# Optimization experiments

Measured on AMD Instinct MI355X. Metric: run time of the kernel, lower is better.

## Reference

```python
import jax, jax.numpy as jnp
import numpy as np

EPS = 1e-5
SLOPE = 0.2
K = 20
B, N = 8, 2048

def _lrelu(x):
    return jnp.where(x >= 0, x, SLOPE * x)

def _bn(x, g, b, m, v, axis):
    # eval-mode batchnorm with running stats
    shape = [1] * x.ndim
    shape[axis] = -1
    g, b, m, v = (t.reshape(shape) for t in (g, b, m, v))
    return g * (x - m) * jax.lax.rsqrt(v + EPS) + b

def _knn(x, k):
    # x: (B, C, N) -> neighbor indices (B, N, k) by largest negative sq dist
    xx = jnp.sum(x * x, axis=1)                      # (B, N)
    inner = jnp.einsum('bcn,bcm->bnm', x, x)         # (B, N, N)
    pd = 2.0 * inner - xx[:, :, None] - xx[:, None, :]
    return jax.lax.top_k(pd, k)[1]

def _graph_feature(x, k):
    # x: (B, C, N) -> (B, 2C, N, k) edge features [nbr - center, center]
    idx = _knn(x, k)                                  # (B, N, k)
    xt = jnp.transpose(x, (0, 2, 1))                  # (B, N, C)
    nbr = xt[jnp.arange(x.shape[0])[:, None, None], idx]  # (B, N, k, C)
    center = xt[:, :, None, :]
    f = jnp.concatenate([nbr - center, jnp.broadcast_to(center, nbr.shape)], axis=-1)
    return jnp.transpose(f, (0, 3, 1, 2))

def _edge_block(x, W, g, b, m, v):
    f = _graph_feature(x, K)                          # (B, 2C, N, k)
    h = jnp.einsum('oc,bcnk->bonk', W, f)             # 1x1 conv
    return jnp.max(_lrelu(_bn(h, g, b, m, v, 1)), axis=-1)

def _forward(x, W1, bn1_g, bn1_b, bn1_m, bn1_v, W2, bn2_g, bn2_b, bn2_m, bn2_v, W3, bn3_g, bn3_b, bn3_m, bn3_v, W4, bn4_g, bn4_b, bn4_m, bn4_v, l1_w, l1_b, bn5_g, bn5_b, bn5_m, bn5_v, l2_w, l2_b, bn6_g, bn6_b, bn6_m, bn6_v, l3_w, l3_b):
    xc = jnp.transpose(x, (0, 2, 1))                  # (B, 3, N)
    x1 = _edge_block(xc, W1, bn1_g, bn1_b, bn1_m, bn1_v)   # (B, 64, N)
    x2 = _edge_block(x1, W2, bn2_g, bn2_b, bn2_m, bn2_v)   # (B, 64, N)
    x3 = _edge_block(x2, W3, bn3_g, bn3_b, bn3_m, bn3_v)   # (B, 128, N)
    h = jnp.concatenate([x1, x2, x3], axis=1)         # (B, 256, N)
    h = _lrelu(_bn(jnp.einsum('oc,bcn->bon', W4, h), bn4_g, bn4_b, bn4_m, bn4_v, 1))
    h = jnp.max(h, axis=-1)                           # (B, 1024)
    h = _lrelu(_bn(h @ l1_w.T + l1_b, bn5_g, bn5_b, bn5_m, bn5_v, 1))
    h = _lrelu(_bn(h @ l2_w.T + l2_b, bn6_g, bn6_b, bn6_m, bn6_v, 1))
    return h @ l3_w.T + l3_b                          # (B, 2)

def setup_inputs() -> dict:
    key = jax.random.key(0)
    ks = iter(jax.random.split(key, 64))
    def rn(shape, s=1.0):
        return jax.random.normal(next(ks), shape, jnp.float32) * s
    def add_bn(inp, prefix, c):
        inp[prefix + '_g'] = jax.random.uniform(next(ks), (c,), jnp.float32, 0.5, 1.5)
        inp[prefix + '_b'] = rn((c,), 0.1)
        inp[prefix + '_m'] = rn((c,), 0.1)
        inp[prefix + '_v'] = jax.random.uniform(next(ks), (c,), jnp.float32, 0.5, 1.5)
    inp = {'x': rn((B, N, 3))}
    inp['W1'] = rn((64, 6), 0.3); add_bn(inp, 'bn1', 64)
    inp['W2'] = rn((64, 128), 0.1); add_bn(inp, 'bn2', 64)
    inp['W3'] = rn((128, 128), 0.1); add_bn(inp, 'bn3', 128)
    inp['W4'] = rn((1024, 256), 0.08); add_bn(inp, 'bn4', 1024)
    inp['l1_w'] = rn((512, 1024), 0.03); inp['l1_b'] = rn((512,), 0.01); add_bn(inp, 'bn5', 512)
    inp['l2_w'] = rn((256, 512), 0.05); inp['l2_b'] = rn((256,), 0.01); add_bn(inp, 'bn6', 256)
    inp['l3_w'] = rn((2, 256), 0.06); inp['l3_b'] = rn((2,), 0.01)
    return inp

def reference(x, W1, bn1_g, bn1_b, bn1_m, bn1_v, W2, bn2_g, bn2_b, bn2_m, bn2_v, W3, bn3_g, bn3_b, bn3_m, bn3_v, W4, bn4_g, bn4_b, bn4_m, bn4_v, l1_w, l1_b, bn5_g, bn5_b, bn5_m, bn5_v, l2_w, l2_b, bn6_g, bn6_b, bn6_m, bn6_v, l3_w, l3_b):
    return _forward(x, W1, bn1_g, bn1_b, bn1_m, bn1_v, W2, bn2_g, bn2_b, bn2_m, bn2_v, W3, bn3_g, bn3_b, bn3_m, bn3_v, W4, bn4_g, bn4_b, bn4_m, bn4_v, l1_w, l1_b, bn5_g, bn5_b, bn5_m, bn5_v, l2_w, l2_b, bn6_g, bn6_b, bn6_m, bn6_v, l3_w, l3_b)
```

## Files before the change

kernel.cpp:

```cpp
#include <hip/hip_runtime.h>
#include <math.h>

#define NN 2048
#define KK 20
#define EPSF 1e-5f

__device__ __forceinline__ float lrelu(float v){ return v >= 0.f ? v : 0.2f*v; }

__device__ __forceinline__ void topk20_insert(float d, int idc, float (&v)[KK], int (&id)[KK]){
#pragma unroll
  for (int j = KK-1; j >= 1; --j){
    bool cjm1 = d > v[j-1];
    bool cj   = d > v[j];
    float nv = cjm1 ? v[j-1] : (cj ? d   : v[j]);
    int   ni = cjm1 ? id[j-1] : (cj ? idc : id[j]);
    v[j] = nv; id[j] = ni;
  }
  if (d > v[0]) { v[0] = d; id[0] = idc; }
}

__global__ void k_prep1(const float* __restrict__ x, const float* __restrict__ W1,
                        float* __restrict__ Y, float* __restrict__ T, float* __restrict__ SQ){
  __shared__ float wa[64][3], wd[64][3];
  int t = threadIdx.x;
  if (t < 64){
#pragma unroll
    for (int c=0;c<3;c++){
      float a = W1[t*6+c], b2 = W1[t*6+3+c];
      wa[t][c] = a; wd[t][c] = b2 - a;
    }
  }
  __syncthreads();
  int gid = blockIdx.x*256 + t;
  int b = gid >> 11, n = gid & (NN-1);
  float px = x[gid*3+0], py = x[gid*3+1], pz = x[gid*3+2];
  SQ[gid] = px*px + py*py + pz*pz;
  float* yb = Y + ((size_t)b*128)*NN + n;
  float* tb = T + ((size_t)b*128)*NN + n;
#pragma unroll 8
  for (int o=0;o<64;o++){
    yb[(size_t)o*NN] = wa[o][0]*px + wa[o][1]*py + wa[o][2]*pz;
    tb[(size_t)o*NN] = wd[o][0]*px + wd[o][1]*py + wd[o][2]*pz;
  }
}

__global__ __launch_bounds__(256) void k_knn3_part(const float* __restrict__ x, const float* __restrict__ SQ,
                                                   float* __restrict__ PV, unsigned short* __restrict__ PI){
  __shared__ __align__(16) unsigned char smem[30720];
  float* cd = (float*)smem;
  float* VL = (float*)smem;
  unsigned short* IL = (unsigned short*)(smem + 20480);
  int t = threadIdx.x;
  int bx = blockIdx.x;
  int cs = bx & 1, nb = bx >> 1;
  int b = blockIdx.y;
  int n_base = nb * 32;
  int cbase = cs * 1024;
  int ql = t & 31, sp = t >> 5;
  int n = n_base + ql;
  int gq = b*NN + n;
  float qx = x[gq*3], qy = x[gq*3+1], qz = x[gq*3+2];
  float qs = SQ[gq];
  float v[KK]; int id[KK];
#pragma unroll
  for (int i=0;i<KK;i++){ v[i] = -INFINITY; id[i] = 0; }
  int mlo = sp * 16;
  for (int tile=0; tile<8; ++tile){
    int m0 = cbase + tile * 128;
    __syncthreads();
#pragma unroll
    for (int i=0;i<2;i++){
      int f2 = t + i*256;
      int m = f2 >> 2, ch = f2 & 3;
      int gm = b*NN + m0 + m;
      cd[f2] = (ch < 3) ? x[gm*3 + ch] : SQ[gm];
    }
    __syncthreads();
    for (int j=mlo; j<mlo+16; ++j){
      float4 c4 = *(const float4*)&cd[j*4];
      float d = 2.f*(qx*c4.x + qy*c4.y + qz*c4.z) - qs - c4.w;
      if (d > v[KK-1]) topk20_insert(d, m0 + j, v, id);
    }
  }
  __syncthreads();
#pragma unroll
  for (int k2=0;k2<KK;k2++){
    VL[(ql*8+sp)*KK + k2] = v[k2];
    IL[(ql*8+sp)*KK + k2] = (unsigned short)id[k2];
  }
  __syncthreads();
  if (t < 32){
    float hv[8]; int hi_[8]; int hp[8];
#pragma unroll
    for (int s=0;s<8;s++){ hp[s]=0; hv[s]=VL[(t*8+s)*KK]; hi_[s]=(int)IL[(t*8+s)*KK]; }
    int nq = n_base + t;
    for (int r=0;r<KK;r++){
      float bv = hv[0]; int bi = hi_[0]; int bs = 0;
#pragma unroll
      for (int s=1;s<8;s++){
        bool win = (hv[s] > bv) || ((hv[s] == bv) && (hi_[s] < bi));
        bv = win ? hv[s] : bv; bi = win ? hi_[s] : bi; bs = win ? s : bs;
      }
      PV[(((size_t)b*2 + cs)*KK + r)*NN + nq] = bv;
      PI[(((size_t)b*2 + cs)*KK + r)*NN + nq] = (unsigned short)bi;
#pragma unroll
      for (int s=0;s<8;s++){
        if (s == bs){
          int np = hp[s] + 1; hp[s] = np;
          bool ok = np < KK;
          hv[s]  = ok ? VL[(t*8+s)*KK + np] : -INFINITY;
          hi_[s] = ok ? (int)IL[(t*8+s)*KK + np] : 0x7FFFFFFF;
        }
      }
    }
  }
}

__global__ void k_sqnorm(const float* __restrict__ X, float* __restrict__ SQ){
  int gid = blockIdx.x*256 + threadIdx.x;
  int b = gid >> 11, n = gid & (NN-1);
  const float* xb = X + (size_t)b*256*NN;
  float s = 0.f;
#pragma unroll
  for (int c=0;c<64;c++){ float vv = xb[(size_t)c*NN + n]; s += vv*vv; }
  SQ[gid] = s;
}

__global__ __launch_bounds__(256) void k_knn64_part(const float* __restrict__ X, const float* __restrict__ SQ,
                                                    float* __restrict__ PV, unsigned short* __restrict__ PI){
  __shared__ __align__(16) unsigned char smem[35328];
  float* cd = (float*)smem;
  float* cs_ = (float*)(smem + 34816);
  float* VL = (float*)smem;
  unsigned short* IL = (unsigned short*)(smem + 20480);
  int t = threadIdx.x;
  int bx = blockIdx.x;
  int cs = bx & 1, nb = bx >> 1;
  int b = blockIdx.y;
  int n_base = nb * 32;
  int cbase = cs * 1024;
  int ql = t & 31, sp = t >> 5;
  int n = n_base + ql;
  const float* xb = X + (size_t)b*256*NN;
  float q[64];
#pragma unroll
  for (int c=0;c<64;c++) q[c] = xb[(size_t)c*NN + n];
  float qs = SQ[b*NN + n];
  float v[KK]; int id[KK];
#pragma unroll
  for (int i=0;i<KK;i++){ v[i]=-INFINITY; id[i]=0; }
  int mlo = sp * 16;
  for (int tile=0; tile<8; ++tile){
    int m0 = cbase + tile*128;
    __syncthreads();
#pragma unroll
    for (int i=0;i<32;i++){
      int flat = i*256 + t;
      int c = flat >> 7, m = flat & 127;
      cd[m*68 + c] = xb[(size_t)c*NN + m0 + m];
    }
    if (t < 128) cs_[t] = SQ[b*NN + m0 + t];
    __syncthreads();
    for (int j=mlo; j<mlo+16; ++j){
      const float* crow = cd + j*68;
      float d = 0.f;
#pragma unroll
      for (int c=0;c<64;c+=4){
        float4 c4 = *(const float4*)&crow[c];
        d += q[c]*c4.x + q[c+1]*c4.y + q[c+2]*c4.z + q[c+3]*c4.w;
      }
      d = 2.f*d - qs - cs_[j];
      if (d > v[KK-1]) topk20_insert(d, m0 + j, v, id);
    }
  }
  __syncthreads();
#pragma unroll
  for (int k2=0;k2<KK;k2++){
    VL[(ql*8+sp)*KK + k2] = v[k2];
    IL[(ql*8+sp)*KK + k2] = (unsigned short)id[k2];
  }
  __syncthreads();
  if (t < 32){
    float hv[8]; int hi_[8]; int hp[8];
#pragma unroll
    for (int s=0;s<8;s++){ hp[s]=0; hv[s]=VL[(t*8+s)*KK]; hi_[s]=(int)IL[(t*8+s)*KK]; }
    int nq = n_base + t;
    for (int r=0;r<KK;r++){
      float bv = hv[0]; int bi = hi_[0]; int bs = 0;
#pragma unroll
      for (int s=1;s<8;s++){
        bool win = (hv[s] > bv) || ((hv[s] == bv) && (hi_[s] < bi));
        bv = win ? hv[s] : bv; bi = win ? hi_[s] : bi; bs = win ? s : bs;
      }
      PV[(((size_t)b*2 + cs)*KK + r)*NN + nq] = bv;
      PI[(((size_t)b*2 + cs)*KK + r)*NN + nq] = (unsigned short)bi;
#pragma unroll
      for (int s=0;s<8;s++){
        if (s == bs){
          int np = hp[s] + 1; hp[s] = np;
          bool ok = np < KK;
          hv[s]  = ok ? VL[(t*8+s)*KK + np] : -INFINITY;
          hi_[s] = ok ? (int)IL[(t*8+s)*KK + np] : 0x7FFFFFFF;
        }
      }
    }
  }
}

__global__ void k_topk_merge(const float* __restrict__ PV, const unsigned short* __restrict__ PI,
                             int* __restrict__ IDX){
  int gid = blockIdx.x*256 + threadIdx.x;
  int b = gid >> 11, n = gid & (NN-1);
  float av[KK], bv[KK]; int ai[KK], bi[KK];
#pragma unroll
  for (int k=0;k<KK;k++){
    av[k] = PV[(((size_t)b*2+0)*KK + k)*NN + n];
    ai[k] = (int)PI[(((size_t)b*2+0)*KK + k)*NN + n];
    bv[k] = PV[(((size_t)b*2+1)*KK + k)*NN + n];
    bi[k] = (int)PI[(((size_t)b*2+1)*KK + k)*NN + n];
  }
  int p0=0, p1=0;
  for (int r=0;r<KK;r++){
    float a = av[p0], bb = bv[p1];
    int ia = ai[p0], ib = bi[p1];
    bool w1 = (bb > a) || ((bb == a) && (ib < ia));
    IDX[((size_t)b*KK + r)*NN + n] = w1 ? ib : ia;
    if (w1) ++p1; else ++p0;
  }
}

__global__ __launch_bounds__(256) void k_edge_apply(const float* __restrict__ Y, const float* __restrict__ T,
                             const int* __restrict__ IDX,
                             const float* __restrict__ g, const float* __restrict__ be,
                             const float* __restrict__ mu, const float* __restrict__ va,
                             float* __restrict__ OUT, int c_off){
  int t = threadIdx.x;
  int nl = t & 127, oh = t >> 7;
  int n = blockIdx.x*128 + nl;
  int b = blockIdx.z;
  int o0 = blockIdx.y*32 + oh*16;
  int idx[KK];
#pragma unroll
  for (int k2=0;k2<KK;k2++) idx[k2] = IDX[((size_t)b*KK + k2)*NN + n];
  for (int oo=0;oo<16;oo++){
    int o = o0 + oo;
    const float* yrow = Y + ((size_t)b*128 + o)*NN;
    float M = -INFINITY;
#pragma unroll
    for (int k2=0;k2<KK;k2++) M = fmaxf(M, yrow[idx[k2]]);
    float s = g[o] * rsqrtf(va[o] + EPSF);
    float val = s*(M + T[((size_t)b*128 + o)*NN + n] - mu[o]) + be[o];
    OUT[((size_t)b*256 + c_off + o)*NN + n] = lrelu(val);
  }
}

template<int O>
__global__ __launch_bounds__(256) void k_yt_gemm(const float* __restrict__ X, const float* __restrict__ W,
                                                 float* __restrict__ Y, float* __restrict__ T){
  __shared__ __align__(16) float wa[O][64];
  __shared__ __align__(16) float wd[O][64];
  int t = threadIdx.x;
  for (int i=t; i<O*64; i+=256){
    int o = i >> 6, c = i & 63;
    float a = W[o*128 + c];
    wa[o][c] = a;
    wd[o][c] = W[o*128 + 64 + c] - a;
  }
  __syncthreads();
  int half = t >> 7, ln = t & 127;
  int gid = blockIdx.x*128 + ln;
  int b = gid >> 11, n = gid & (NN-1);
  const float* xb = X + (size_t)b*256*NN;
  float q[64];
#pragma unroll
  for (int c=0;c<64;c++) q[c] = xb[(size_t)c*NN + n];
  int o0 = half * (O/2);
  for (int o=o0; o<o0+O/2; ++o){
    float ay=0.f, at=0.f;
#pragma unroll
    for (int c=0;c<64;c+=4){
      float4 a4 = *(const float4*)&wa[o][c];
      float4 d4 = *(const float4*)&wd[o][c];
      ay += a4.x*q[c] + a4.y*q[c+1] + a4.z*q[c+2] + a4.w*q[c+3];
      at += d4.x*q[c] + d4.y*q[c+1] + d4.z*q[c+2] + d4.w*q[c+3];
    }
    Y[((size_t)b*128 + o)*NN + n] = ay;
    T[((size_t)b*128 + o)*NN + n] = at;
  }
}

__global__ __launch_bounds__(256) void k_w4t(const float* __restrict__ W4, float* __restrict__ W4T){
  __shared__ float Tt[64][65];
  int t = threadIdx.x;
  int c0 = blockIdx.x * 64, o0 = blockIdx.y * 64;
#pragma unroll
  for (int p=0;p<16;p++){
    int f = p*256 + t;
    int i = f >> 6, j = f & 63;
    Tt[i][j] = W4[(size_t)(o0+i)*256 + c0 + j];
  }
  __syncthreads();
#pragma unroll
  for (int p=0;p<16;p++){
    int f = p*256 + t;
    int i = f >> 6, j = f & 63;
    W4T[(size_t)(c0+i)*1024 + o0 + j] = Tt[j][i];
  }
}

__global__ __launch_bounds__(256) void k_w4max(const float* __restrict__ CAT, const float* __restrict__ W4T,
                                               float* __restrict__ PART){
  __shared__ __align__(16) float wt[32][132];
  __shared__ __align__(16) float ct[32][132];
  int t = threadIdx.x;
  int io = t >> 4, in_ = t & 15;
  int nb = blockIdx.x * 128, ob = blockIdx.y * 128, b = blockIdx.z;
  const float* catb = CAT + (size_t)b*256*NN;
  float acc[8][8];
#pragma unroll
  for (int r=0;r<8;r++)
#pragma unroll
    for (int c=0;c<8;c++) acc[r][c]=0.f;
  for (int c0=0; c0<256; c0+=32){
    __syncthreads();
#pragma unroll
    for (int p=0;p<4;p++){
      int idx = p*256 + t;
      int cc = idx >> 5, o4 = (idx & 31) * 4;
      *(float4*)&wt[cc][o4] = *(const float4*)&W4T[(size_t)(c0+cc)*1024 + ob + o4];
    }
#pragma unroll
    for (int p=0;p<4;p++){
      int idx = p*256 + t;
      int cc = idx >> 5, n4 = (idx & 31) * 4;
      *(float4*)&ct[cc][n4] = *(const float4*)&catb[(size_t)(c0+cc)*NN + nb + n4];
    }
    __syncthreads();
#pragma unroll 4
    for (int c=0;c<32;c++){
      float4 a0 = *(const float4*)&wt[c][io*8];
      float4 a1 = *(const float4*)&wt[c][io*8+4];
      float4 b0 = *(const float4*)&ct[c][in_*8];
      float4 b1 = *(const float4*)&ct[c][in_*8+4];
      float ar[8] = {a0.x,a0.y,a0.z,a0.w,a1.x,a1.y,a1.z,a1.w};
      float br[8] = {b0.x,b0.y,b0.z,b0.w,b1.x,b1.y,b1.z,b1.w};
#pragma unroll
      for (int r=0;r<8;r++)
#pragma unroll
        for (int s=0;s<8;s++) acc[r][s] += ar[r]*br[s];
    }
  }
#pragma unroll
  for (int r=0;r<8;r++){
    float m = acc[r][0];
#pragma unroll
    for (int s=1;s<8;s++) m = fmaxf(m, acc[r][s]);
    m = fmaxf(m, __shfl_xor(m, 1));
    m = fmaxf(m, __shfl_xor(m, 2));
    m = fmaxf(m, __shfl_xor(m, 4));
    m = fmaxf(m, __shfl_xor(m, 8));
    if (in_ == 0){
      int o = ob + io*8 + r;
      PART[((size_t)b*1024 + o)*16 + blockIdx.x] = m;
    }
  }
}

__global__ void k_reduce4(const float* __restrict__ PART,
                          const float* __restrict__ g, const float* __restrict__ be,
                          const float* __restrict__ mu, const float* __restrict__ va,
                          float* __restrict__ H4){
  int gid = blockIdx.x*256 + threadIdx.x;
  int o = gid & 1023;
  float M = -INFINITY;
#pragma unroll
  for (int i=0;i<16;i++) M = fmaxf(M, PART[(size_t)gid*16 + i]);
  float s = g[o]*rsqrtf(va[o]+EPSF);
  H4[gid] = lrelu(s*(M - mu[o]) + be[o]);
}

__global__ __launch_bounds__(256) void k_mlp(const float* __restrict__ H4,
      const float* __restrict__ l1w, const float* __restrict__ l1b,
      const float* __restrict__ g5, const float* __restrict__ b5,
      const float* __restrict__ m5, const float* __restrict__ v5,
      const float* __restrict__ l2w, const float* __restrict__ l2b,
      const float* __restrict__ g6, const float* __restrict__ b6,
      const float* __restrict__ m6, const float* __restrict__ v6,
      const float* __restrict__ l3w, const float* __restrict__ l3b,
      float* __restrict__ out){
  __shared__ float h[1024];
  __shared__ float h5[512];
  __shared__ float h6[256];
  int b = blockIdx.x, t = threadIdx.x;
  for (int i=t;i<1024;i+=256) h[i] = H4[b*1024+i];
  __syncthreads();
  for (int o=t;o<512;o+=256){
    float acc = l1b[o];
    for (int c=0;c<1024;c+=4){
      float4 w = *(const float4*)&l1w[(size_t)o*1024 + c];
      acc += w.x*h[c] + w.y*h[c+1] + w.z*h[c+2] + w.w*h[c+3];
    }
    float s = g5[o]*rsqrtf(v5[o]+EPSF);
    h5[o] = lrelu(s*(acc - m5[o]) + b5[o]);
  }
  __syncthreads();
  if (t < 256){
    int o = t;
    float acc = l2b[o];
    for (int c=0;c<512;c+=4){
      float4 w = *(const float4*)&l2w[(size_t)o*512 + c];
      acc += w.x*h5[c] + w.y*h5[c+1] + w.z*h5[c+2] + w.w*h5[c+3];
    }
    float s = g6[o]*rsqrtf(v6[o]+EPSF);
    h6[o] = lrelu(s*(acc - m6[o]) + b6[o]);
  }
  __syncthreads();
  if (t < 128){
    int o = t >> 6, l = t & 63;
    float p = 0.f;
#pragma unroll
    for (int j=0;j<4;j++){ int c = j*64 + l; p += l3w[o*256 + c]*h6[c]; }
    p += __shfl_xor(p, 32); p += __shfl_xor(p, 16); p += __shfl_xor(p, 8);
    p += __shfl_xor(p, 4);  p += __shfl_xor(p, 2);  p += __shfl_xor(p, 1);
    if (l == 0) out[b*2 + o] = p + l3b[o];
  }
}

extern "C" void kernel_launch(void* const* d_in, const int* in_sizes, int n_in,
                              void* d_out, int out_size, void* d_ws, size_t ws_size,
                              hipStream_t stream){
  (void)in_sizes; (void)n_in; (void)out_size; (void)ws_size;
  const float* x    = (const float*)d_in[0];
  const float* W1   = (const float*)d_in[1];
  const float* bn1g = (const float*)d_in[2];
  const float* bn1b = (const float*)d_in[3];
  const float* bn1m = (const float*)d_in[4];
  const float* bn1v = (const float*)d_in[5];
  const float* W2   = (const float*)d_in[6];
  const float* bn2g = (const float*)d_in[7];
  const float* bn2b = (const float*)d_in[8];
  const float* bn2m = (const float*)d_in[9];
  const float* bn2v = (const float*)d_in[10];
  const float* W3   = (const float*)d_in[11];
  const float* bn3g = (const float*)d_in[12];
  const float* bn3b = (const float*)d_in[13];
  const float* bn3m = (const float*)d_in[14];
  const float* bn3v = (const float*)d_in[15];
  const float* W4   = (const float*)d_in[16];
  const float* bn4g = (const float*)d_in[17];
  const float* bn4b = (const float*)d_in[18];
  const float* bn4m = (const float*)d_in[19];
  const float* bn4v = (const float*)d_in[20];
  const float* l1w  = (const float*)d_in[21];
  const float* l1b  = (const float*)d_in[22];
  const float* bn5g = (const float*)d_in[23];
  const float* bn5b = (const float*)d_in[24];
  const float* bn5m = (const float*)d_in[25];
  const float* bn5v = (const float*)d_in[26];
  const float* l2w  = (const float*)d_in[27];
  const float* l2b  = (const float*)d_in[28];
  const float* bn6g = (const float*)d_in[29];
  const float* bn6b = (const float*)d_in[30];
  const float* bn6m = (const float*)d_in[31];
  const float* bn6v = (const float*)d_in[32];
  const float* l3w  = (const float*)d_in[33];
  const float* l3b  = (const float*)d_in[34];

  float* CAT  = (float*)d_ws;
  float* Yb   = CAT + (size_t)8*256*NN;
  float* Tb   = Yb  + (size_t)8*128*NN;
  float* SQ   = Tb  + (size_t)8*128*NN;
  int*   IDX  = (int*)(SQ + (size_t)8*NN);
  float* PART = (float*)(IDX + (size_t)8*KK*NN);
  float* H4   = PART + (size_t)8*1024*16;
  float* W4T  = H4 + (size_t)8*1024;
  float* PTV  = W4T + (size_t)256*1024;
  unsigned short* PTI = (unsigned short*)(PTV + (size_t)8*2*KK*NN);

  k_w4t<<<dim3(4,16),256,0,stream>>>(W4, W4T);
  k_prep1<<<64,256,0,stream>>>(x, W1, Yb, Tb, SQ);
  k_knn3_part<<<dim3(128,8),256,0,stream>>>(x, SQ, PTV, PTI);
  k_topk_merge<<<64,256,0,stream>>>(PTV, PTI, IDX);
  k_edge_apply<<<dim3(16,2,8),256,0,stream>>>(Yb, Tb, IDX, bn1g, bn1b, bn1m, bn1v, CAT, 0);
  k_sqnorm<<<64,256,0,stream>>>(CAT, SQ);
  k_knn64_part<<<dim3(128,8),256,0,stream>>>(CAT, SQ, PTV, PTI);
  k_topk_merge<<<64,256,0,stream>>>(PTV, PTI, IDX);
  k_yt_gemm<64><<<128,256,0,stream>>>(CAT, W2, Yb, Tb);
  k_edge_apply<<<dim3(16,2,8),256,0,stream>>>(Yb, Tb, IDX, bn2g, bn2b, bn2m, bn2v, CAT, 64);
  k_sqnorm<<<64,256,0,stream>>>(CAT + (size_t)64*NN, SQ);
  k_knn64_part<<<dim3(128,8),256,0,stream>>>(CAT + (size_t)64*NN, SQ, PTV, PTI);
  k_topk_merge<<<64,256,0,stream>>>(PTV, PTI, IDX);
  k_yt_gemm<128><<<128,256,0,stream>>>(CAT + (size_t)64*NN, W3, Yb, Tb);
  k_edge_apply<<<dim3(16,4,8),256,0,stream>>>(Yb, Tb, IDX, bn3g, bn3b, bn3m, bn3v, CAT, 128);
  k_w4max<<<dim3(16,8,8),256,0,stream>>>(CAT, W4T, PART);
  k_reduce4<<<32,256,0,stream>>>(PART, bn4g, bn4b, bn4m, bn4v, H4);
  k_mlp<<<8,256,0,stream>>>(H4, l1w, l1b, bn5g, bn5b, bn5m, bn5v,
                            l2w, l2b, bn6g, bn6b, bn6m, bn6v, l3w, l3b, (float*)d_out);
}
```

Measured before the change: 1.506 ms.

## Move in-block top-k merge to a global 16-way merge kernel

The kNN partial kernels no longer merge the 8 per-thread top-20 lists inside the block through shared memory. Each thread now writes its own list to global memory, and a new merge kernel does a 16-way merge per query. This cuts shared memory use (the 64-dim kernel also shrinks its candidate tile from 128 to 64 columns) and adds a launch-bounds occupancy hint, aiming for more resident blocks. In exchange, partial-result traffic to global memory grows eightfold and the merge kernel does more uncoalesced dependent loads.

New measurement: 2.908 ms. +93.1%, slower.

```diff
diff --git a/kernel.cpp b/kernel.cpp
--- a/kernel.cpp
+++ b/kernel.cpp
@@ -44,18 +44,14 @@
   }
 }
 
-__global__ __launch_bounds__(256) void k_knn3_part(const float* __restrict__ x, const float* __restrict__ SQ,
-                                                   float* __restrict__ PV, unsigned short* __restrict__ PI){
-  __shared__ __align__(16) unsigned char smem[30720];
-  float* cd = (float*)smem;
-  float* VL = (float*)smem;
-  unsigned short* IL = (unsigned short*)(smem + 20480);
-  int t = threadIdx.x;
-  int bx = blockIdx.x;
-  int cs = bx & 1, nb = bx >> 1;
+__global__ __launch_bounds__(256,4) void k_knn3_part(const float* __restrict__ x, const float* __restrict__ SQ,
+                                                     float* __restrict__ PV, unsigned short* __restrict__ PI){
+  __shared__ __align__(16) float cd[128*4];
+  int t = threadIdx.x;
+  int half = blockIdx.x & 1, nb = blockIdx.x >> 1;
   int b = blockIdx.y;
   int n_base = nb * 32;
-  int cbase = cs * 1024;
+  int cbase = half * 1024;
   int ql = t & 31, sp = t >> 5;
   int n = n_base + ql;
   int gq = b*NN + n;
@@ -82,37 +78,11 @@
       if (d > v[KK-1]) topk20_insert(d, m0 + j, v, id);
     }
   }
-  __syncthreads();
-#pragma unroll
-  for (int k2=0;k2<KK;k2++){
-    VL[(ql*8+sp)*KK + k2] = v[k2];
-    IL[(ql*8+sp)*KK + k2] = (unsigned short)id[k2];
-  }
-  __syncthreads();
-  if (t < 32){
-    float hv[8]; int hi_[8]; int hp[8];
-#pragma unroll
-    for (int s=0;s<8;s++){ hp[s]=0; hv[s]=VL[(t*8+s)*KK]; hi_[s]=(int)IL[(t*8+s)*KK]; }
-    int nq = n_base + t;
-    for (int r=0;r<KK;r++){
-      float bv = hv[0]; int bi = hi_[0]; int bs = 0;
-#pragma unroll
-      for (int s=1;s<8;s++){
-        bool win = (hv[s] > bv) || ((hv[s] == bv) && (hi_[s] < bi));
-        bv = win ? hv[s] : bv; bi = win ? hi_[s] : bi; bs = win ? s : bs;
-      }
-      PV[(((size_t)b*2 + cs)*KK + r)*NN + nq] = bv;
-      PI[(((size_t)b*2 + cs)*KK + r)*NN + nq] = (unsigned short)bi;
-#pragma unroll
-      for (int s=0;s<8;s++){
-        if (s == bs){
-          int np = hp[s] + 1; hp[s] = np;
-          bool ok = np < KK;
-          hv[s]  = ok ? VL[(t*8+s)*KK + np] : -INFINITY;
-          hi_[s] = ok ? (int)IL[(t*8+s)*KK + np] : 0x7FFFFFFF;
-        }
-      }
-    }
+  size_t base = ((size_t)b*16 + half*8 + sp)*KK;
+#pragma unroll
+  for (int r=0;r<KK;r++){
+    PV[(base + r)*NN + n] = v[r];
+    PI[(base + r)*NN + n] = (unsigned short)id[r];
   }
 }
 
@@ -126,19 +96,15 @@
   SQ[gid] = s;
 }
 
-__global__ __launch_bounds__(256) void k_knn64_part(const float* __restrict__ X, const float* __restrict__ SQ,
-                                                    float* __restrict__ PV, unsigned short* __restrict__ PI){
-  __shared__ __align__(16) unsigned char smem[35328];
-  float* cd = (float*)smem;
-  float* cs_ = (float*)(smem + 34816);
-  float* VL = (float*)smem;
-  unsigned short* IL = (unsigned short*)(smem + 20480);
-  int t = threadIdx.x;
-  int bx = blockIdx.x;
-  int cs = bx & 1, nb = bx >> 1;
+__global__ __launch_bounds__(256,4) void k_knn64_part(const float* __restrict__ X, const float* __restrict__ SQ,
+                                                      float* __restrict__ PV, unsigned short* __restrict__ PI){
+  __shared__ __align__(16) float cd[64*68];
+  __shared__ float cs_[64];
+  int t = threadIdx.x;
+  int half = blockIdx.x & 1, nb = blockIdx.x >> 1;
   int b = blockIdx.y;
   int n_base = nb * 32;
-  int cbase = cs * 1024;
+  int cbase = half * 1024;
   int ql = t & 31, sp = t >> 5;
   int n = n_base + ql;
   const float* xb = X + (size_t)b*256*NN;
@@ -149,19 +115,19 @@
   float v[KK]; int id[KK];
 #pragma unroll
   for (int i=0;i<KK;i++){ v[i]=-INFINITY; id[i]=0; }
-  int mlo = sp * 16;
-  for (int tile=0; tile<8; ++tile){
-    int m0 = cbase + tile*128;
-    __syncthreads();
-#pragma unroll
-    for (int i=0;i<32;i++){
+  int jlo = sp * 8;
+  for (int tile=0; tile<16; ++tile){
+    int m0 = cbase + tile*64;
+    __syncthreads();
+#pragma unroll
+    for (int i=0;i<16;i++){
       int flat = i*256 + t;
-      int c = flat >> 7, m = flat & 127;
+      int c = flat >> 6, m = flat & 63;
       cd[m*68 + c] = xb[(size_t)c*NN + m0 + m];
     }
-    if (t < 128) cs_[t] = SQ[b*NN + m0 + t];
-    __syncthreads();
-    for (int j=mlo; j<mlo+16; ++j){
+    if (t < 64) cs_[t] = SQ[b*NN + m0 + t];
+    __syncthreads();
+    for (int j=jlo; j<jlo+8; ++j){
       const float* crow = cd + j*68;
       float d = 0.f;
 #pragma unroll
@@ -173,59 +139,42 @@
       if (d > v[KK-1]) topk20_insert(d, m0 + j, v, id);
     }
   }
-  __syncthreads();
-#pragma unroll
-  for (int k2=0;k2<KK;k2++){
-    VL[(ql*8+sp)*KK + k2] = v[k2];
-    IL[(ql*8+sp)*KK + k2] = (unsigned short)id[k2];
-  }
-  __syncthreads();
-  if (t < 32){
-    float hv[8]; int hi_[8]; int hp[8];
-#pragma unroll
-    for (int s=0;s<8;s++){ hp[s]=0; hv[s]=VL[(t*8+s)*KK]; hi_[s]=(int)IL[(t*8+s)*KK]; }
-    int nq = n_base + t;
-    for (int r=0;r<KK;r++){
-      float bv = hv[0]; int bi = hi_[0]; int bs = 0;
-#pragma unroll
-      for (int s=1;s<8;s++){
-        bool win = (hv[s] > bv) || ((hv[s] == bv) && (hi_[s] < bi));
-        bv = win ? hv[s] : bv; bi = win ? hi_[s] : bi; bs = win ? s : bs;
-      }
-      PV[(((size_t)b*2 + cs)*KK + r)*NN + nq] = bv;
-      PI[(((size_t)b*2 + cs)*KK + r)*NN + nq] = (unsigned short)bi;
-#pragma unroll
-      for (int s=0;s<8;s++){
-        if (s == bs){
-          int np = hp[s] + 1; hp[s] = np;
-          bool ok = np < KK;
-          hv[s]  = ok ? VL[(t*8+s)*KK + np] : -INFINITY;
-          hi_[s] = ok ? (int)IL[(t*8+s)*KK + np] : 0x7FFFFFFF;
-        }
-      }
-    }
-  }
-}
-
-__global__ void k_topk_merge(const float* __restrict__ PV, const unsigned short* __restrict__ PI,
-                             int* __restrict__ IDX){
+  size_t base = ((size_t)b*16 + half*8 + sp)*KK;
+#pragma unroll
+  for (int r=0;r<KK;r++){
+    PV[(base + r)*NN + n] = v[r];
+    PI[(base + r)*NN + n] = (unsigned short)id[r];
+  }
+}
+
+__global__ void k_topk_merge16(const float* __restrict__ PV, const unsigned short* __restrict__ PI,
+                               int* __restrict__ IDX){
   int gid = blockIdx.x*256 + threadIdx.x;
   int b = gid >> 11, n = gid & (NN-1);
-  float av[KK], bv[KK]; int ai[KK], bi[KK];
-#pragma unroll
-  for (int k=0;k<KK;k++){
-    av[k] = PV[(((size_t)b*2+0)*KK + k)*NN + n];
-    ai[k] = (int)PI[(((size_t)b*2+0)*KK + k)*NN + n];
-    bv[k] = PV[(((size_t)b*2+1)*KK + k)*NN + n];
-    bi[k] = (int)PI[(((size_t)b*2+1)*KK + k)*NN + n];
-  }
-  int p0=0, p1=0;
+  float hv[16]; int hi_[16]; int hp[16];
+#pragma unroll
+  for (int s=0;s<16;s++){
+    hp[s] = 0;
+    hv[s] = PV[(((size_t)b*16 + s)*KK)*NN + n];
+    hi_[s] = (int)PI[(((size_t)b*16 + s)*KK)*NN + n];
+  }
   for (int r=0;r<KK;r++){
-    float a = av[p0], bb = bv[p1];
-    int ia = ai[p0], ib = bi[p1];
-    bool w1 = (bb > a) || ((bb == a) && (ib < ia));
-    IDX[((size_t)b*KK + r)*NN + n] = w1 ? ib : ia;
-    if (w1) ++p1; else ++p0;
+    float bv = hv[0]; int bi = hi_[0]; int bs = 0;
+#pragma unroll
+    for (int s=1;s<16;s++){
+      bool win = (hv[s] > bv) || ((hv[s] == bv) && (hi_[s] < bi));
+      bv = win ? hv[s] : bv; bi = win ? hi_[s] : bi; bs = win ? s : bs;
+    }
+    IDX[((size_t)b*KK + r)*NN + n] = bi;
+#pragma unroll
+    for (int s=0;s<16;s++){
+      if (s == bs){
+        int np = hp[s] + 1; hp[s] = np;
+        bool ok = np < KK;
+        hv[s]  = ok ? PV[(((size_t)b*16 + s)*KK + np)*NN + n] : -INFINITY;
+        hi_[s] = ok ? (int)PI[(((size_t)b*16 + s)*KK + np)*NN + n] : 0x7FFFFFFF;
+      }
+    }
   }
 }
 
@@ -475,21 +424,21 @@
   float* H4   = PART + (size_t)8*1024*16;
   float* W4T  = H4 + (size_t)8*1024;
   float* PTV  = W4T + (size_t)256*1024;
-  unsigned short* PTI = (unsigned short*)(PTV + (size_t)8*2*KK*NN);
+  unsigned short* PTI = (unsigned short*)(PTV + (size_t)8*16*KK*NN);
 
   k_w4t<<<dim3(4,16),256,0,stream>>>(W4, W4T);
   k_prep1<<<64,256,0,stream>>>(x, W1, Yb, Tb, SQ);
   k_knn3_part<<<dim3(128,8),256,0,stream>>>(x, SQ, PTV, PTI);
-  k_topk_merge<<<64,256,0,stream>>>(PTV, PTI, IDX);
+  k_topk_merge16<<<64,256,0,stream>>>(PTV, PTI, IDX);
   k_edge_apply<<<dim3(16,2,8),256,0,stream>>>(Yb, Tb, IDX, bn1g, bn1b, bn1m, bn1v, CAT, 0);
   k_sqnorm<<<64,256,0,stream>>>(CAT, SQ);
   k_knn64_part<<<dim3(128,8),256,0,stream>>>(CAT, SQ, PTV, PTI);
-  k_topk_merge<<<64,256,0,stream>>>(PTV, PTI, IDX);
+  k_topk_merge16<<<64,256,0,stream>>>(PTV, PTI, IDX);
   k_yt_gemm<64><<<128,256,0,stream>>>(CAT, W2, Yb, Tb);
   k_edge_apply<<<dim3(16,2,8),256,0,stream>>>(Yb, Tb, IDX, bn2g, bn2b, bn2m, bn2v, CAT, 64);
   k_sqnorm<<<64,256,0,stream>>>(CAT + (size_t)64*NN, SQ);
   k_knn64_part<<<dim3(128,8),256,0,stream>>>(CAT + (size_t)64*NN, SQ, PTV, PTI);
-  k_topk_merge<<<64,256,0,stream>>>(PTV, PTI, IDX);
+  k_topk_merge16<<<64,256,0,stream>>>(PTV, PTI, IDX);
   k_yt_gemm<128><<<128,256,0,stream>>>(CAT + (size_t)64*NN, W3, Yb, Tb);
   k_edge_apply<<<dim3(16,4,8),256,0,stream>>>(Yb, Tb, IDX, bn3g, bn3b, bn3m, bn3v, CAT, 128);
   k_w4max<<<dim3(16,8,8),256,0,stream>>>(CAT, W4T, PART);
```
